# Performance work log

Hardware: AMD Instinct MI355X
Metric: run time of the kernel (lower is better)

## Reference

```python
import jax, jax.numpy as jnp
import numpy as np

EMBED_DIM = 512
NUM_HEADS = 8
B, L_Q, L_K = 2, 2048, 2048


def setup_inputs() -> dict:
    key = jax.random.key(0)
    ks = jax.random.split(key, 8)
    s = 0.02  # weight init scale
    return {
        "query": jax.random.normal(ks[0], (B, L_Q, EMBED_DIM), jnp.float32),
        "key":   jax.random.normal(ks[1], (B, L_K, EMBED_DIM), jnp.float32),
        "value": jax.random.normal(ks[2], (B, L_K, EMBED_DIM), jnp.float32),
        "wq": jax.random.normal(ks[3], (EMBED_DIM, EMBED_DIM), jnp.float32) * s,
        "wk": jax.random.normal(ks[4], (EMBED_DIM, EMBED_DIM), jnp.float32) * s,
        "wv": jax.random.normal(ks[5], (EMBED_DIM, EMBED_DIM), jnp.float32) * s,
        "bq": jnp.zeros((EMBED_DIM,), jnp.float32),
        "bk": jnp.zeros((EMBED_DIM,), jnp.float32),
        "bv": jnp.zeros((EMBED_DIM,), jnp.float32),
        "wo": jax.random.normal(ks[6], (EMBED_DIM, EMBED_DIM), jnp.float32) * s,
        "bo": jnp.zeros((EMBED_DIM,), jnp.float32),
    }


def _prob_sparse_mask(query, key, num_heads):
    # Faithful to _prob_QK: max-mean sparsity score, top-k query selection,
    # gather of reduced queries, reduced QK matmul (vectorized, no python loops).
    Bq, Lq, D = query.shape
    Lk = key.shape[1]
    dh = D // num_heads
    n_top = int(np.log(Lk))  # int(np.ceil/np.log) as in source forward: int(np.log(L_K))
    Q = query.reshape(Bq, Lq, num_heads, dh)
    K = key.reshape(Bq, Lk, num_heads, dh)
    Qh = jnp.transpose(Q, (0, 2, 1, 3))                      # [B,H,Lq,dh]
    # NOTE: source does K.transpose(1,2).reshape(B,H,D,L_K) -- a reshape, not a
    # transpose of the last two dims. We replicate that exactly.
    Kr = jnp.transpose(K, (0, 2, 1, 3)).reshape(Bq, num_heads, dh, Lk)  # [B,H,dh,Lk]
    QK = jnp.einsum('bhqd,bhdk->bhqk', Qh, Kr)               # [B,H,Lq,Lk]
    M = QK.max(-1) - QK.sum(-1) / Lk                         # max-mean score [B,H,Lq]
    _, M_top = jax.lax.top_k(M, n_top)                       # [B,H,n_top]
    Q_red = jnp.take_along_axis(Qh, M_top[..., None], axis=2)  # [B,H,n_top,dh]
    QK_red = jnp.einsum('bhtd,bhdk->bhtk', Q_red, Kr)        # [B,H,n_top,Lk]
    # Scatter reduced rows back into a full additive attn mask (zeros elsewhere).
    mask = jnp.zeros((Bq, num_heads, Lq, Lk), QK.dtype)
    bi = jnp.arange(Bq)[:, None, None]
    hi = jnp.arange(num_heads)[None, :, None]
    return mask.at[bi, hi, M_top].set(QK_red)


def reference(query, key, value, wq, wk, wv, bq, bk, bv, wo, bo):
    Bq, Lq, D = query.shape
    Lk = key.shape[1]
    H = NUM_HEADS
    dh = D // H
    mask = _prob_sparse_mask(query, key, H)                  # [B,H,Lq,Lk]
    q = (query @ wq.T + bq).reshape(Bq, Lq, H, dh).transpose(0, 2, 1, 3)
    k = (key @ wk.T + bk).reshape(Bq, Lk, H, dh).transpose(0, 2, 1, 3)
    v = (value @ wv.T + bv).reshape(Bq, Lk, H, dh).transpose(0, 2, 1, 3)
    scores = jnp.einsum('bhqd,bhkd->bhqk', q, k) * (dh ** -0.5) + mask
    attn = jax.nn.softmax(scores, axis=-1)                   # dropout inactive (eval)
    out = jnp.einsum('bhqk,bhkd->bhqd', attn, v)
    out = out.transpose(0, 2, 1, 3).reshape(Bq, Lq, D)
    return out @ wo.T + bo
```

## Files before the change

### kernel.cpp

```cpp
#include <hip/hip_runtime.h>
#include <type_traits>

#define DEV static __device__ __forceinline__

typedef short s16;
typedef __attribute__((ext_vector_type(4))) short short4_t;
typedef __attribute__((ext_vector_type(8))) short short8;
typedef __attribute__((ext_vector_type(4))) float f32x4;
typedef __attribute__((ext_vector_type(16))) float f32x16;

#define NB 2
#define NH 8
#define SL 2048
#define DM 512
#define DH 64
#define NTOP 7
#define LOG2E 1.4426950408889634f
#define NROWS (NB*NH*SL)
#define FSPLIT 4
#define SSPLIT 4

DEV short f2bf(float x){
  union { float f; unsigned u; } v; v.f = x;
  unsigned r = v.u + 0x7fffu + ((v.u >> 16) & 1u);
  return (short)(r >> 16);
}
DEV float bf2f(short b){
  union { float f; unsigned u; } v; v.u = ((unsigned)(unsigned short)b) << 16;
  return v.f;
}
DEV f32x4 mfma16(short8 a, short8 b, f32x4 c){
  return __builtin_amdgcn_mfma_f32_16x16x32_bf16(a, b, c, 0, 0, 0);
}
DEV f32x16 mfma32(short8 a, short8 b, f32x16 c){
  return __builtin_amdgcn_mfma_f32_32x32x16_bf16(a, b, c, 0, 0, 0);
}
DEV unsigned cvtpk(float lo, float hi){
  unsigned r;
  asm("v_cvt_pk_bf16_f32 %0, %1, %2" : "=v"(r) : "v"(lo), "v"(hi));
  return r;
}
DEV void gl2lds16(const s16* g, s16* l){
  __builtin_amdgcn_global_load_lds(
      (const __attribute__((address_space(1))) unsigned*)g,
      (__attribute__((address_space(3))) unsigned*)l, 16, 0, 0);
}

__global__ void prep_kernel(const float* __restrict__ query, const float* __restrict__ key,
    const float* __restrict__ value,
    const float* __restrict__ wq, const float* __restrict__ wk,
    const float* __restrict__ wv, const float* __restrict__ wo,
    s16* __restrict__ q_hi, s16* __restrict__ q_lo, s16* __restrict__ xk, s16* __restrict__ xv,
    s16* __restrict__ khi, s16* __restrict__ klo,
    s16* __restrict__ wqb, s16* __restrict__ wkb, s16* __restrict__ wvb, s16* __restrict__ wob){
  const int nbb = (NB*SL*DM)/256;
  const int wbb = (DM*DM)/256;
  __shared__ s16 thi[64][66];
  __shared__ s16 tlo[64][66];
  int bid = blockIdx.x;
  int t = threadIdx.x;
  if (bid < nbb){
    int i = bid*256 + t;
    float v = query[i];
    short h = f2bf(v);
    q_hi[i] = h;
    q_lo[i] = f2bf(v - bf2f(h));
    return;
  }
  bid -= nbb;
  if (bid < nbb){ int i = bid*256 + t; xk[i] = f2bf(key[i]); return; }
  bid -= nbb;
  if (bid < nbb){ int i = bid*256 + t; xv[i] = f2bf(value[i]); return; }
  bid -= nbb;
  if (bid < 512){
    int k6 = bid & 31, h = (bid >> 5) & 7, b = bid >> 8;
    int kl = t & 63, dq = t >> 6;
    #pragma unroll
    for (int dd = 0; dd < 16; ++dd){
      int d = dd*4 + dq;
      float v = key[((size_t)b*SL + d*32 + k6)*DM + h*DH + kl];
      short hh = f2bf(v);
      thi[d][kl] = hh;
      tlo[d][kl] = f2bf(v - bf2f(hh));
    }
    __syncthreads();
    int d2 = t & 63, kq = t >> 6;
    size_t obase = (((size_t)(b*NH + h))*SL + (size_t)k6*64)*DH;
    #pragma unroll
    for (int kk = 0; kk < 16; ++kk){
      int kl2 = kk*4 + kq;
      khi[obase + (size_t)kl2*DH + d2] = thi[d2][kl2];
      klo[obase + (size_t)kl2*DH + d2] = tlo[d2][kl2];
    }
    return;
  }
  bid -= 512;
  if (bid < wbb){ int i = bid*256 + t; wqb[i] = f2bf(wq[i]); return; }
  bid -= wbb;
  if (bid < wbb){ int i = bid*256 + t; wkb[i] = f2bf(wk[i]); return; }
  bid -= wbb;
  if (bid < wbb){ int i = bid*256 + t; wvb[i] = f2bf(wv[i]); return; }
  bid -= wbb;
  if (bid < wbb){ int i = bid*256 + t; wob[i] = f2bf(wo[i]); return; }
}

__global__ __launch_bounds__(256) void vpt_kernel(const s16* __restrict__ Vp, s16* __restrict__ VpT){
  __shared__ s16 tl[64][66];
  int bid = blockIdx.x;
  int k6 = bid & 31, h = (bid >> 5) & 7, b = bid >> 8;
  int t = threadIdx.x;
  int d = t & 63, kq = t >> 6;
  #pragma unroll
  for (int kk = 0; kk < 16; ++kk){
    int kl = kk*4 + kq;
    tl[kl][d] = Vp[((size_t)b*SL + k6*64 + kl)*DM + h*DH + d];
  }
  __syncthreads();
  int kl2 = t & 63, dq = t >> 6;
  size_t obase = ((size_t)(b*NH + h))*DH*SL + (size_t)k6*64;
  #pragma unroll
  for (int dd = 0; dd < 16; ++dd){
    int d2 = dd*4 + dq;
    VpT[obase + (size_t)d2*SL + kl2] = tl[kl2][d2];
  }
}

template<int OUTF32>
DEV void gemm_body(const s16* __restrict__ A, const s16* __restrict__ Bw,
        const float* __restrict__ bias, void* __restrict__ Cout, int bid, int tid, float scale){
  __shared__ __align__(16) s16 Abuf[2][128*64];
  __shared__ __align__(16) s16 Bbuf[2][64*64];
  int nt = bid >> 3, ot = bid & 7;
  int w = tid >> 6, l = tid & 63;
  int lr = l & 15, lg = l >> 4;
  int n0 = nt*128, o0 = ot*64;
  auto stage = [&](int cur, int kg){
    #pragma unroll
    for (int i = 0; i < 4; ++i){
      int r = w*32 + i*8 + (l>>3);
      int cs = (l&7) ^ (r&7);
      gl2lds16(A + (size_t)(n0 + r)*DM + kg + cs*8, &Abuf[cur][(w*32 + i*8)*64]);
    }
    #pragma unroll
    for (int i = 0; i < 2; ++i){
      int r = w*16 + i*8 + (l>>3);
      int cs = (l&7) ^ (r&7);
      gl2lds16(Bw + (size_t)(o0 + r)*DM + kg + cs*8, &Bbuf[cur][(w*16 + i*8)*64]);
    }
  };
  f32x4 acc[2][4] = {};
  stage(0, 0);
  __syncthreads();
  const int NIT = DM/64;
  for (int it = 0; it < NIT; ++it){
    int cur = it & 1;
    if (it + 1 < NIT) stage(cur^1, (it+1)*64);
    #pragma unroll
    for (int kc = 0; kc < 2; ++kc){
      short8 a0 = *(const short8*)&Abuf[cur][(w*32 +      lr)*64 + ((kc*4+lg) ^ (lr&7))*8];
      short8 a1 = *(const short8*)&Abuf[cur][(w*32 + 16 + lr)*64 + ((kc*4+lg) ^ (lr&7))*8];
      #pragma unroll
      for (int c = 0; c < 4; ++c){
        short8 bf = *(const short8*)&Bbuf[cur][(c*16 + lr)*64 + ((kc*4+lg) ^ (lr&7))*8];
        acc[0][c] = mfma16(a0, bf, acc[0][c]);
        acc[1][c] = mfma16(a1, bf, acc[1][c]);
      }
    }
    __syncthreads();
  }
  #pragma unroll
  for (int sub = 0; sub < 2; ++sub)
    #pragma unroll
    for (int c = 0; c < 4; ++c){
      int col = o0 + c*16 + lr;
      float bb = bias[col];
      #pragma unroll
      for (int j = 0; j < 4; ++j){
        int row = n0 + w*32 + sub*16 + lg*4 + j;
        float v = (acc[sub][c][j] + bb)*scale;
        if (OUTF32) ((float*)Cout)[(size_t)row*DM + col] = v;
        else        ((s16*) Cout)[(size_t)row*DM + col] = f2bf(v);
      }
    }
}

__global__ __launch_bounds__(256) void gemm_proj(const s16* __restrict__ Aq, const s16* __restrict__ Ak,
        const s16* __restrict__ Av, const s16* __restrict__ Wq, const s16* __restrict__ Wk,
        const s16* __restrict__ Wv, const float* __restrict__ bq, const float* __restrict__ bk,
        const float* __restrict__ bv, s16* __restrict__ Oq, s16* __restrict__ Ok, s16* __restrict__ Ov){
  int which = blockIdx.x >> 8;
  const s16* A  = which == 0 ? Aq : which == 1 ? Ak : Av;
  const s16* Bw = which == 0 ? Wq : which == 1 ? Wk : Wv;
  const float* bias = which == 0 ? bq : which == 1 ? bk : bv;
  s16* C = which == 0 ? Oq : which == 1 ? Ok : Ov;
  float scale = which == 0 ? 0.125f*LOG2E : 1.0f;
  gemm_body<0>(A, Bw, bias, C, blockIdx.x & 255, threadIdx.x, scale);
}

__global__ __launch_bounds__(256) void gemm_out(const s16* __restrict__ A, const s16* __restrict__ Bw,
        const float* __restrict__ bias, float* __restrict__ Cout){
  gemm_body<1>(A, Bw, bias, Cout, blockIdx.x, threadIdx.x, 1.0f);
}

__global__ __launch_bounds__(512) void stats_kernel(const s16* __restrict__ qhi, const s16* __restrict__ qlo,
        const s16* __restrict__ khi, const s16* __restrict__ klo,
        float* __restrict__ Mmx, float* __restrict__ Msm){
  __shared__ __align__(16) s16 Hbuf[2][64*64];
  __shared__ __align__(16) s16 Lbuf[2][64*64];
  int bid = blockIdx.x;
  int s = bid & 3, qt = (bid >> 2) & 15, h = (bid >> 6) & 7, b = bid >> 9;
  int tid = threadIdx.x;
  int w = tid >> 6, l = tid & 63;
  int lr = l & 15, lg = l >> 4;
  int dx = lr & 7;
  int q0 = qt*128 + w*16;
  const s16* qp  = qhi + ((size_t)b*SL + q0 + lr)*DM + h*DH + lg*8;
  const s16* qlp = qlo + ((size_t)b*SL + q0 + lr)*DM + h*DH + lg*8;
  short8 qh0 = *(const short8*)qp;
  short8 qh1 = *(const short8*)(qp + 32);
  short8 ql0 = *(const short8*)qlp;
  short8 ql1 = *(const short8*)(qlp + 32);
  const s16* kb  = khi + ((size_t)b*NH + h)*SL*DH;
  const s16* klb = klo + ((size_t)b*NH + h)*SL*DH;
  const s16* hR0 = &Hbuf[0][lr*64 + ((lg      ^ dx)*8)];
  const s16* hR1 = &Hbuf[0][lr*64 + (((4+lg) ^ dx)*8)];
  const s16* lR0 = &Lbuf[0][lr*64 + ((lg      ^ dx)*8)];
  const s16* lR1 = &Lbuf[0][lr*64 + (((4+lg) ^ dx)*8)];
  int rS = tid >> 3;
  int csK = (tid & 7) ^ (rS & 7);
  auto stage = [&](int cur, int kg){
    gl2lds16(kb  + (size_t)(kg + rS)*DH + csK*8, &Hbuf[cur][w*512]);
    gl2lds16(klb + (size_t)(kg + rS)*DH + csK*8, &Lbuf[cur][w*512]);
  };
  float mx = -1e30f, sm = 0.f;
  auto body = [&](auto CURC){
    constexpr int CUR = decltype(CURC)::value;
    #pragma unroll
    for (int t = 0; t < 4; ++t){
      short8 kh0 = *(const short8*)(hR0 + CUR*4096 + t*1024);
      short8 kh1 = *(const short8*)(hR1 + CUR*4096 + t*1024);
      short8 kl0 = *(const short8*)(lR0 + CUR*4096 + t*1024);
      short8 kl1 = *(const short8*)(lR1 + CUR*4096 + t*1024);
      f32x4 sacc = {};
      sacc = mfma16(kh0, qh0, sacc);
      sacc = mfma16(kh1, qh1, sacc);
      sacc = mfma16(kl0, qh0, sacc);
      sacc = mfma16(kl1, qh1, sacc);
      sacc = mfma16(kh0, ql0, sacc);
      sacc = mfma16(kh1, ql1, sacc);
      #pragma unroll
      for (int j = 0; j < 4; ++j){ mx = fmaxf(mx, sacc[j]); sm += sacc[j]; }
    }
  };
  int kbeg = s*(SL/SSPLIT);
  const int NI2 = (SL/SSPLIT)/128;
  stage(0, kbeg);
  __syncthreads();
  #pragma unroll 1
  for (int i2 = 0; i2 < NI2; ++i2){
    stage(1, kbeg + (2*i2+1)*64);
    body(std::integral_constant<int,0>{});
    __syncthreads();
    if (i2 < NI2-1) stage(0, kbeg + (2*i2+2)*64);
    body(std::integral_constant<int,1>{});
    __syncthreads();
  }
  mx = fmaxf(mx, __shfl_xor(mx, 16));
  mx = fmaxf(mx, __shfl_xor(mx, 32));
  sm += __shfl_xor(sm, 16);
  sm += __shfl_xor(sm, 32);
  if (lg == 0){
    size_t row = ((size_t)b*NH + h)*SL + q0 + lr;
    Mmx[(size_t)s*NROWS + row] = mx;
    Msm[(size_t)s*NROWS + row] = sm;
  }
}

__global__ __launch_bounds__(256) void topk_kernel(const float* __restrict__ Mmx,
        const float* __restrict__ Msm, int* __restrict__ topidx, int* __restrict__ rowsel){
  int bh = blockIdx.x;
  int t = threadIdx.x;
  int w = t >> 6, l = t & 63;
  __shared__ float smv[SL];
  __shared__ float rv[4];
  __shared__ int   ri[4];
  size_t base = (size_t)bh*SL;
  for (int i = t; i < SL; i += 256){
    float mx = Mmx[base + i];
    float sm = Msm[base + i];
    #pragma unroll
    for (int s = 1; s < SSPLIT; ++s){
      mx = fmaxf(mx, Mmx[(size_t)s*NROWS + base + i]);
      sm += Msm[(size_t)s*NROWS + base + i];
    }
    smv[i] = mx - sm*(1.0f/SL);
    rowsel[base + i] = -1;
  }
  __syncthreads();
  for (int tt = 0; tt < NTOP; ++tt){
    float bvv = -1e38f; int bi = SL;
    for (int i = t; i < SL; i += 256){
      float v = smv[i];
      if (v > bvv){ bvv = v; bi = i; }
    }
    #pragma unroll
    for (int off = 32; off >= 1; off >>= 1){
      float ov = __shfl_xor(bvv, off);
      int oi = __shfl_xor(bi, off);
      if (ov > bvv || (ov == bvv && oi < bi)){ bvv = ov; bi = oi; }
    }
    if (l == 0){ rv[w] = bvv; ri[w] = bi; }
    __syncthreads();
    if (t == 0){
      float bv2 = rv[0]; int bi2 = ri[0];
      #pragma unroll
      for (int ww = 1; ww < 4; ++ww)
        if (rv[ww] > bv2 || (rv[ww] == bv2 && ri[ww] < bi2)){ bv2 = rv[ww]; bi2 = ri[ww]; }
      topidx[bh*8 + tt] = bi2;
      rowsel[base + bi2] = tt;
      smv[bi2] = -1e38f;
    }
    __syncthreads();
  }
}

__global__ __launch_bounds__(256) void maskrow_kernel(const float* __restrict__ query,
        const float* __restrict__ key, const int* __restrict__ topidx, float* __restrict__ maskrows){
  __shared__ float tile[64][65];
  __shared__ float qs[NTOP][64];
  int bid = blockIdx.x;
  int k6 = bid & 31, h = (bid >> 5) & 7, b = bid >> 8;
  int bh = b*NH + h;
  int t = threadIdx.x;
  int kl = t & 63, w = t >> 6;
  for (int i = t; i < NTOP*64; i += 256){
    int tt = i >> 6, d = i & 63;
    qs[tt][d] = query[((size_t)b*SL + topidx[bh*8 + tt])*DM + h*DH + d];
  }
  #pragma unroll
  for (int dd = 0; dd < 16; ++dd){
    int d = dd*4 + w;
    tile[d][kl] = key[((size_t)b*SL + d*32 + k6)*DM + h*DH + kl];
  }
  __syncthreads();
  for (int tt = w; tt < NTOP; tt += 4){
    float acc = 0.f;
    #pragma unroll
    for (int d = 0; d < 64; ++d)
      acc = fmaf(qs[tt][d], tile[d][kl], acc);
    maskrows[((size_t)bh*NTOP + tt)*SL + k6*64 + kl] = acc*LOG2E;
  }
}

__global__ __launch_bounds__(256, 3) void flash_kernel(const s16* __restrict__ Qp,
        const s16* __restrict__ Kp, const s16* __restrict__ VpT,
        const float* __restrict__ maskrows, const int* __restrict__ rowsel,
        float* __restrict__ Opart, float* __restrict__ lpart){
  __shared__ __align__(16) s16 SB[4*64*64];
  int bid = blockIdx.x;
  int s = bid & 3, qt = (bid >> 2) & 15, h = (bid >> 6) & 7, b = bid >> 9;
  int tid = threadIdx.x;
  int w = tid >> 6, l = tid & 63;
  int ln = l & 31, lh = l >> 5;
  int q0 = qt*128 + w*32;
  int bh = b*NH + h;
  const s16* qp = Qp + ((size_t)b*SL + q0 + ln)*DM + h*DH + lh*8;
  short8 bq[4];
  #pragma unroll
  for (int kc = 0; kc < 4; ++kc) bq[kc] = *(const short8*)(qp + kc*16);
  int sel = rowsel[(size_t)bh*SL + q0 + ln];
  const float* mrow = maskrows + ((size_t)bh*NTOP + (sel >= 0 ? sel : 0))*SL;
  const s16* kpb = Kp + (size_t)b*SL*DM + h*DH;
  const s16* vtb = VpT + (size_t)bh*DH*SL;
  const s16* kR[2][4];
  #pragma unroll
  for (int g = 0; g < 2; ++g)
    #pragma unroll
    for (int kc = 0; kc < 4; ++kc)
      kR[g][kc] = &SB[(g*32 + ln)*64 + (((kc*2 + lh) ^ (ln & 7))*8)];
  int rS8 = l >> 3;
  int csS = (l & 7) ^ (rS8 & 7);
  auto stage = [&](int cur, int kg){
    #pragma unroll
    for (int c = 0; c < 2; ++c){
      int r = c*32 + w*8 + rS8;
      gl2lds16(kpb + (size_t)(kg + r)*DM + csS*8, &SB[(size_t)cur*4096 + (c*32 + w*8)*64]);
      gl2lds16(vtb + (size_t)r*SL + kg + csS*8, &SB[8192 + (size_t)cur*4096 + (c*32 + w*8)*64]);
    }
  };
  f32x16 accO[2] = {};
  float ls0 = 0.f, ls1 = 0.f, ls2 = 0.f, ls3 = 0.f;
  auto body = [&](auto CURC, int k0){
    constexpr int CB = decltype(CURC)::value * 8192;
    f32x16 S[2] = {};
    #pragma unroll
    for (int g = 0; g < 2; ++g)
      #pragma unroll
      for (int kc = 0; kc < 4; ++kc){
        short8 kf = *(const short8*)((const char*)kR[g][kc] + CB);
        S[g] = mfma32(kf, bq[kc], S[g]);
      }
    if (sel >= 0){
      #pragma unroll
      for (int g = 0; g < 2; ++g)
        #pragma unroll
        for (int rq = 0; rq < 4; ++rq)
          #pragma unroll
          for (int j = 0; j < 4; ++j)
            S[g][rq*4 + j] += mrow[k0 + g*32 + rq*8 + lh*4 + j];
    }
    #pragma unroll
    for (int g = 0; g < 2; ++g)
      #pragma unroll
      for (int rq = 0; rq < 4; ++rq){
        S[g][rq*4+0] = exp2f(S[g][rq*4+0]); ls0 += S[g][rq*4+0];
        S[g][rq*4+1] = exp2f(S[g][rq*4+1]); ls1 += S[g][rq*4+1];
        S[g][rq*4+2] = exp2f(S[g][rq*4+2]); ls2 += S[g][rq*4+2];
        S[g][rq*4+3] = exp2f(S[g][rq*4+3]); ls3 += S[g][rq*4+3];
      }
    unsigned W[2][8];
    #pragma unroll
    for (int g = 0; g < 2; ++g)
      #pragma unroll
      for (int t = 0; t < 8; ++t)
        W[g][t] = cvtpk(S[g][2*t], S[g][2*t+1]);
    short8 pf[4];
    #pragma unroll
    for (int kc = 0; kc < 4; ++kc){
      int g = kc >> 1, j = kc & 1;
      unsigned a0 = W[g][4*j + 0], a1 = W[g][4*j + 2];
      asm("v_permlane32_swap_b32 %0, %1" : "+v"(a0), "+v"(a1));
      unsigned b0 = W[g][4*j + 1], b1 = W[g][4*j + 3];
      asm("v_permlane32_swap_b32 %0, %1" : "+v"(b0), "+v"(b1));
      union { unsigned u[4]; short8 s8; } uu;
      uu.u[0] = a0; uu.u[1] = b0; uu.u[2] = a1; uu.u[3] = b1;
      pf[kc] = uu.s8;
    }
    #pragma unroll
    for (int dg = 0; dg < 2; ++dg)
      #pragma unroll
      for (int kc = 0; kc < 4; ++kc){
        short8 vf = *(const short8*)((const char*)kR[dg][kc] + CB + 16384);
        accO[dg] = mfma32(vf, pf[kc], accO[dg]);
      }
  };
  int kbeg = s*(SL/FSPLIT);
  const int NI2 = (SL/FSPLIT)/128;
  stage(0, kbeg);
  __syncthreads();
  #pragma unroll 1
  for (int i2 = 0; i2 < NI2; ++i2){
    stage(1, kbeg + (2*i2+1)*64);
    body(std::integral_constant<int,0>{}, kbeg + 2*i2*64);
    __syncthreads();
    if (i2 < NI2-1) stage(0, kbeg + (2*i2+2)*64);
    body(std::integral_constant<int,1>{}, kbeg + (2*i2+1)*64);
    __syncthreads();
  }
  float lsum = (ls0 + ls1) + (ls2 + ls3);
  lsum += __shfl_xor(lsum, 32);
  size_t row = (size_t)bh*SL + q0 + ln;
  float* Op = Opart + ((size_t)s*NROWS + row)*DH;
  #pragma unroll
  for (int dg = 0; dg < 2; ++dg)
    #pragma unroll
    for (int rq = 0; rq < 4; ++rq){
      f32x4 v = { accO[dg][rq*4+0], accO[dg][rq*4+1], accO[dg][rq*4+2], accO[dg][rq*4+3] };
      *(f32x4*)(Op + dg*32 + rq*8 + lh*4) = v;
    }
  if (lh == 0)
    lpart[(size_t)s*NROWS + row] = lsum;
}

__global__ __launch_bounds__(256) void flash_combine(const float* __restrict__ Opart,
        const float* __restrict__ lpart, s16* __restrict__ outh){
  int row = blockIdx.x*4 + (threadIdx.x >> 6);
  int d = threadIdx.x & 63;
  float L = 0.f, o = 0.f;
  #pragma unroll
  for (int s = 0; s < FSPLIT; ++s){
    L += lpart[(size_t)s*NROWS + row];
    o += Opart[((size_t)s*NROWS + row)*DH + d];
  }
  o /= L;
  int b = row >> 14, h = (row >> 11) & 7, q = row & (SL - 1);
  outh[((size_t)b*SL + q)*DM + h*DH + d] = f2bf(o);
}

extern "C" void kernel_launch(void* const* d_in, const int* in_sizes, int n_in,
                              void* d_out, int out_size, void* d_ws, size_t ws_size,
                              hipStream_t stream){
  (void)in_sizes; (void)n_in; (void)out_size;
  const float* query = (const float*)d_in[0];
  const float* key   = (const float*)d_in[1];
  const float* value = (const float*)d_in[2];
  const float* wq    = (const float*)d_in[3];
  const float* wk    = (const float*)d_in[4];
  const float* wv    = (const float*)d_in[5];
  const float* bq    = (const float*)d_in[6];
  const float* bk    = (const float*)d_in[7];
  const float* bv    = (const float*)d_in[8];
  const float* wo    = (const float*)d_in[9];
  const float* bo    = (const float*)d_in[10];

  const size_t NE = (size_t)NB*SL*DM;
  const size_t WE = (size_t)DM*DM;

  char* p = (char*)d_ws;
  size_t off = 0;
  auto alloc = [&](size_t n)->char*{ char* r = p + off; off += (n + 255) & ~(size_t)255; return r; };
  s16* wob = (s16*)alloc(WE*2);
  s16* Qp  = (s16*)alloc(NE*2);
  s16* Kp  = (s16*)alloc(NE*2);
  s16* VpT = (s16*)alloc(NE*2);
  float* maskrows = (float*)alloc((size_t)NB*NH*NTOP*SL*4);
  int* topidx   = (int*)alloc((size_t)NB*NH*8*4);
  int* rowsel   = (int*)alloc((size_t)NROWS*4);
  float* Mmx    = (float*)alloc((size_t)SSPLIT*NROWS*4);
  float* Msm    = (float*)alloc((size_t)SSPLIT*NROWS*4);
  float* lpart  = (float*)alloc((size_t)FSPLIT*NROWS*4);
  float* Opart  = (float*)alloc((size_t)FSPLIT*NROWS*DH*4);
  s16* outh = (s16*)alloc(NE*2);
  s16* q_hi = (s16*)alloc(NE*2);
  s16* q_lo = (s16*)alloc(NE*2);
  s16* xk   = (s16*)alloc(NE*2);
  s16* xv   = (s16*)alloc(NE*2);
  s16* khatT_hi = (s16*)alloc(NE*2);
  s16* khatT_lo = (s16*)alloc(NE*2);
  s16* wqb = (s16*)alloc(WE*2);
  s16* wkb = (s16*)alloc(WE*2);
  s16* wvb = (s16*)alloc(WE*2);
  s16* Vp  = (s16*)alloc(NE*2);
  if (off > ws_size) return;

  const int nbb = (int)(NE/256);
  const int wbb = (int)(WE/256);
  prep_kernel<<<3*nbb + 512 + 4*wbb, 256, 0, stream>>>(query, key, value, wq, wk, wv, wo,
      q_hi, q_lo, xk, xv, khatT_hi, khatT_lo, wqb, wkb, wvb, wob);

  gemm_proj<<<3*256, 256, 0, stream>>>(q_hi, xk, xv, wqb, wkb, wvb, bq, bk, bv, Qp, Kp, Vp);
  vpt_kernel<<<512, 256, 0, stream>>>(Vp, VpT);

  stats_kernel<<<NB*NH*(SL/128)*SSPLIT, 512, 0, stream>>>(q_hi, q_lo, khatT_hi, khatT_lo, Mmx, Msm);
  topk_kernel<<<NB*NH, 256, 0, stream>>>(Mmx, Msm, topidx, rowsel);
  maskrow_kernel<<<512, 256, 0, stream>>>(query, key, topidx, maskrows);

  flash_kernel<<<NB*NH*(SL/128)*FSPLIT, 256, 0, stream>>>(Qp, Kp, VpT, maskrows, rowsel,
      Opart, lpart);
  flash_combine<<<NROWS/4, 256, 0, stream>>>(Opart, lpart, outh);
  gemm_out<<<256, 256, 0, stream>>>(outh, wob, bo, (float*)d_out);
}
```

Before: 140.2 us.

## Register-staged prefetch with full unroll; compute row sums via MFMA and set priorities

Both the score-statistics kernel and the flash-attention kernel stop using direct global-to-LDS loads. Each tile is now loaded into registers two steps ahead and written to the swizzled LDS buffer one step ahead, and the loop over tiles is fully unrolled. In the flash kernel the softmax row sum is computed by an extra MFMA against a vector of bf16 ones instead of scalar adds, and s_setprio brackets the MFMA sections. The goal is more latency hiding and less VALU work, at the cost of extra registers and four more MFMAs per tile, and the row sum is now taken from bf16-rounded probabilities.

```diff
diff --git a/kernel.cpp b/kernel.cpp
--- a/kernel.cpp
+++ b/kernel.cpp
@@ -227,10 +227,19 @@
   const s16* lR0 = &Lbuf[0][lr*64 + ((lg      ^ dx)*8)];
   const s16* lR1 = &Lbuf[0][lr*64 + (((4+lg) ^ dx)*8)];
   int rS = tid >> 3;
-  int csK = (tid & 7) ^ (rS & 7);
-  auto stage = [&](int cur, int kg){
-    gl2lds16(kb  + (size_t)(kg + rS)*DH + csK*8, &Hbuf[cur][w*512]);
-    gl2lds16(klb + (size_t)(kg + rS)*DH + csK*8, &Lbuf[cur][w*512]);
+  int slot = tid & 7;
+  int cs = slot ^ (rS & 7);
+  int kbeg = s*(SL/SSPLIT);
+  const int NT = (SL/SSPLIT)/64;
+  f32x4 hreg, lreg;
+  auto loadr = [&](int t){
+    int kg = kbeg + t*64;
+    hreg = *(const f32x4*)(kb  + (size_t)(kg + rS)*DH + cs*8);
+    lreg = *(const f32x4*)(klb + (size_t)(kg + rS)*DH + cs*8);
+  };
+  auto writer = [&](int buf){
+    *(f32x4*)&Hbuf[buf][rS*64 + slot*8] = hreg;
+    *(f32x4*)&Lbuf[buf][rS*64 + slot*8] = lreg;
   };
   float mx = -1e30f, sm = 0.f;
   auto body = [&](auto CURC){
@@ -252,19 +261,21 @@
       for (int j = 0; j < 4; ++j){ mx = fmaxf(mx, sacc[j]); sm += sacc[j]; }
     }
   };
-  int kbeg = s*(SL/SSPLIT);
-  const int NI2 = (SL/SSPLIT)/128;
-  stage(0, kbeg);
+  loadr(0);
+  writer(0);
+  loadr(1);
   __syncthreads();
-  #pragma unroll 1
-  for (int i2 = 0; i2 < NI2; ++i2){
-    stage(1, kbeg + (2*i2+1)*64);
-    body(std::integral_constant<int,0>{});
+  auto step = [&](auto TC){
+    constexpr int T = decltype(TC)::value;
+    if constexpr (T + 1 < NT) writer((T+1)&1);
+    if constexpr (T + 2 < NT) loadr(T+2);
+    body(std::integral_constant<int, T&1>{});
     __syncthreads();
-    if (i2 < NI2-1) stage(0, kbeg + (2*i2+2)*64);
-    body(std::integral_constant<int,1>{});
-    __syncthreads();
-  }
+  };
+  step(std::integral_constant<int,0>{}); step(std::integral_constant<int,1>{});
+  step(std::integral_constant<int,2>{}); step(std::integral_constant<int,3>{});
+  step(std::integral_constant<int,4>{}); step(std::integral_constant<int,5>{});
+  step(std::integral_constant<int,6>{}); step(std::integral_constant<int,7>{});
   mx = fmaxf(mx, __shfl_xor(mx, 16));
   mx = fmaxf(mx, __shfl_xor(mx, 32));
   sm += __shfl_xor(sm, 16);
@@ -378,21 +389,38 @@
     #pragma unroll
     for (int kc = 0; kc < 4; ++kc)
       kR[g][kc] = &SB[(g*32 + ln)*64 + (((kc*2 + lh) ^ (ln & 7))*8)];
-  int rS8 = l >> 3;
-  int csS = (l & 7) ^ (rS8 & 7);
-  auto stage = [&](int cur, int kg){
+  int r8 = l >> 3;
+  int slot = l & 7;
+  int cs = slot ^ (r8 & 7);
+  int kbeg = s*(SL/FSPLIT);
+  const int NT = (SL/FSPLIT)/64;
+  f32x4 kreg[2], vreg[2];
+  auto loadr = [&](int t){
+    int kg = kbeg + t*64;
     #pragma unroll
     for (int c = 0; c < 2; ++c){
-      int r = c*32 + w*8 + rS8;
-      gl2lds16(kpb + (size_t)(kg + r)*DM + csS*8, &SB[(size_t)cur*4096 + (c*32 + w*8)*64]);
-      gl2lds16(vtb + (size_t)r*SL + kg + csS*8, &SB[8192 + (size_t)cur*4096 + (c*32 + w*8)*64]);
-    }
-  };
+      int r = c*32 + w*8 + r8;
+      kreg[c] = *(const f32x4*)(kpb + (size_t)(kg + r)*DM + cs*8);
+      vreg[c] = *(const f32x4*)(vtb + (size_t)r*SL + kg + cs*8);
+    }
+  };
+  auto writer = [&](int buf){
+    #pragma unroll
+    for (int c = 0; c < 2; ++c){
+      int r = c*32 + w*8 + r8;
+      *(f32x4*)&SB[(size_t)buf*4096 + r*64 + slot*8] = kreg[c];
+      *(f32x4*)&SB[8192 + (size_t)buf*4096 + r*64 + slot*8] = vreg[c];
+    }
+  };
+  short8 ones;
+  #pragma unroll
+  for (int i = 0; i < 8; ++i) ones[i] = (short)0x3F80;
   f32x16 accO[2] = {};
-  float ls0 = 0.f, ls1 = 0.f, ls2 = 0.f, ls3 = 0.f;
+  f32x16 accL = {};
   auto body = [&](auto CURC, int k0){
     constexpr int CB = decltype(CURC)::value * 8192;
     f32x16 S[2] = {};
+    __builtin_amdgcn_s_setprio(1);
     #pragma unroll
     for (int g = 0; g < 2; ++g)
       #pragma unroll
@@ -400,6 +428,7 @@
         short8 kf = *(const short8*)((const char*)kR[g][kc] + CB);
         S[g] = mfma32(kf, bq[kc], S[g]);
       }
+    __builtin_amdgcn_s_setprio(0);
     if (sel >= 0){
       #pragma unroll
       for (int g = 0; g < 2; ++g)
@@ -412,12 +441,8 @@
     #pragma unroll
     for (int g = 0; g < 2; ++g)
       #pragma unroll
-      for (int rq = 0; rq < 4; ++rq){
-        S[g][rq*4+0] = exp2f(S[g][rq*4+0]); ls0 += S[g][rq*4+0];
-        S[g][rq*4+1] = exp2f(S[g][rq*4+1]); ls1 += S[g][rq*4+1];
-        S[g][rq*4+2] = exp2f(S[g][rq*4+2]); ls2 += S[g][rq*4+2];
-        S[g][rq*4+3] = exp2f(S[g][rq*4+3]); ls3 += S[g][rq*4+3];
-      }
+      for (int e = 0; e < 16; ++e)
+        S[g][e] = exp2f(S[g][e]);
     unsigned W[2][8];
     #pragma unroll
     for (int g = 0; g < 2; ++g)
@@ -436,6 +461,10 @@
       uu.u[0] = a0; uu.u[1] = b0; uu.u[2] = a1; uu.u[3] = b1;
       pf[kc] = uu.s8;
     }
+    __builtin_amdgcn_s_setprio(1);
+    #pragma unroll
+    for (int kc = 0; kc < 4; ++kc)
+      accL = mfma32(ones, pf[kc], accL);
     #pragma unroll
     for (int dg = 0; dg < 2; ++dg)
       #pragma unroll
@@ -443,22 +472,23 @@
         short8 vf = *(const short8*)((const char*)kR[dg][kc] + CB + 16384);
         accO[dg] = mfma32(vf, pf[kc], accO[dg]);
       }
-  };
-  int kbeg = s*(SL/FSPLIT);
-  const int NI2 = (SL/FSPLIT)/128;
-  stage(0, kbeg);
+    __builtin_amdgcn_s_setprio(0);
+  };
+  loadr(0);
+  writer(0);
+  loadr(1);
   __syncthreads();
-  #pragma unroll 1
-  for (int i2 = 0; i2 < NI2; ++i2){
-    stage(1, kbeg + (2*i2+1)*64);
-    body(std::integral_constant<int,0>{}, kbeg + 2*i2*64);
+  auto step = [&](auto TC){
+    constexpr int T = decltype(TC)::value;
+    if constexpr (T + 1 < NT) writer((T+1)&1);
+    if constexpr (T + 2 < NT) loadr(T+2);
+    body(std::integral_constant<int, T&1>{}, kbeg + T*64);
     __syncthreads();
-    if (i2 < NI2-1) stage(0, kbeg + (2*i2+2)*64);
-    body(std::integral_constant<int,1>{}, kbeg + (2*i2+1)*64);
-    __syncthreads();
-  }
-  float lsum = (ls0 + ls1) + (ls2 + ls3);
-  lsum += __shfl_xor(lsum, 32);
+  };
+  step(std::integral_constant<int,0>{}); step(std::integral_constant<int,1>{});
+  step(std::integral_constant<int,2>{}); step(std::integral_constant<int,3>{});
+  step(std::integral_constant<int,4>{}); step(std::integral_constant<int,5>{});
+  step(std::integral_constant<int,6>{}); step(std::integral_constant<int,7>{});
   size_t row = (size_t)bh*SL + q0 + ln;
   float* Op = Opart + ((size_t)s*NROWS + row)*DH;
   #pragma unroll
@@ -469,7 +499,7 @@
       *(f32x4*)(Op + dg*32 + rq*8 + lh*4) = v;
     }
   if (lh == 0)
-    lpart[(size_t)s*NROWS + row] = lsum;
+    lpart[(size_t)s*NROWS + row] = accL[0];
 }
 
 __global__ __launch_bounds__(256) void flash_combine(const float* __restrict__ Opart,
```

After: 143.5 us. +2.3%, slower.
